# Kernel tuning notes

Hardware: AMD Instinct MI355X
Metric: run time of the kernel (lower is better)

The kernel has to match this reference:

```python
import jax, jax.numpy as jnp
import numpy as np

POS_TH = 0.5
NEG_TH = 0.4
NEGPOS_RATIO = 3
BBOX_ALPHA = 1.5
CONF_ALPHA = 1.0
VAR_CXCY = 0.1
VAR_WH = 0.2
NUM_CLASSES = 41
B, P, G = 8, 100000, 16


def setup_inputs() -> dict:
    key = jax.random.key(0)
    k = jax.random.split(key, 8)
    loc_data = jax.random.normal(k[0], (B, P, 4), dtype=jnp.float32)
    conf_data = jax.random.normal(k[1], (B, P, NUM_CLASSES), dtype=jnp.float32)
    # priors in (cx, cy, w, h), normalized coords
    p_cxy = jax.random.uniform(k[2], (P, 2), minval=0.0, maxval=1.0)
    p_wh = jax.random.uniform(k[3], (P, 2), minval=0.02, maxval=0.3)
    priors = jnp.concatenate([p_cxy, p_wh], axis=1).astype(jnp.float32)
    # gt boxes in point form (x1, y1, x2, y2)
    g_cxy = jax.random.uniform(k[4], (B, G, 2), minval=0.15, maxval=0.85)
    g_wh = jax.random.uniform(k[5], (B, G, 2), minval=0.05, maxval=0.4)
    gt_boxes = jnp.concatenate([
        jnp.clip(g_cxy - g_wh / 2, 0.0, 1.0),
        jnp.clip(g_cxy + g_wh / 2, 0.0, 1.0),
    ], axis=-1).astype(jnp.float32)
    gt_labels = jax.random.randint(k[6], (B, G), 1, NUM_CLASSES)
    return {"loc_data": loc_data, "conf_data": conf_data, "priors": priors,
            "gt_boxes": gt_boxes, "gt_labels": gt_labels}


def point_form(pr):
    return jnp.concatenate([pr[:, :2] - pr[:, 2:] / 2,
                            pr[:, :2] + pr[:, 2:] / 2], axis=1)


def jaccard(a, b):
    # a: [G,4] xyxy, b: [P,4] xyxy -> [G,P]
    lt = jnp.maximum(a[:, None, :2], b[None, :, :2])
    rb = jnp.minimum(a[:, None, 2:], b[None, :, 2:])
    wh = jnp.clip(rb - lt, 0.0)
    inter = wh[..., 0] * wh[..., 1]
    area_a = ((a[:, 2] - a[:, 0]) * (a[:, 3] - a[:, 1]))[:, None]
    area_b = ((b[:, 2] - b[:, 0]) * (b[:, 3] - b[:, 1]))[None, :]
    return inter / (area_a + area_b - inter)


def encode(matched, priors):
    # matched [P,4] xyxy, priors [P,4] cxcywh -> SSD offsets with variances
    g_cxcy = ((matched[:, :2] + matched[:, 2:]) / 2 - priors[:, :2]) / (VAR_CXCY * priors[:, 2:])
    g_wh = jnp.log(jnp.clip((matched[:, 2:] - matched[:, :2]) / priors[:, 2:], 1e-8)) / VAR_WH
    return jnp.concatenate([g_cxcy, g_wh], axis=1)


def match_one(gt_box, gt_label, priors):
    # gt_box [G,4], gt_label [G], priors [P,4] -> loc_t [P,4], conf_t [P]
    pf = point_form(priors)
    ov = jaccard(gt_box, pf)                      # [G,P]
    best_truth_ov = ov.max(axis=0)                # [P]
    best_truth_idx = ov.argmax(axis=0)            # [P]
    best_prior_idx = ov.argmax(axis=1)            # [G] best prior per gt
    # force-match each gt to its best prior
    best_truth_ov = best_truth_ov.at[best_prior_idx].set(2.0)
    best_truth_idx = best_truth_idx.at[best_prior_idx].set(jnp.arange(gt_box.shape[0]))
    conf = gt_label[best_truth_idx]
    conf = jnp.where(best_truth_ov < POS_TH, -1, conf)   # neutral
    conf = jnp.where(best_truth_ov < NEG_TH, 0, conf)    # background
    loc = encode(gt_box[best_truth_idx], priors)
    return loc, conf


def reference(loc_data, conf_data, priors, gt_boxes, gt_labels):
    bsz, n_pri, n_cls = conf_data.shape
    loc_t, conf_t = jax.vmap(match_one, in_axes=(0, 0, None))(gt_boxes, gt_labels, priors)
    pos = conf_t > 0                               # [B,P]
    num_pos = pos.sum(axis=1)                      # [B]
    # pos_weights: uniform 1/num_pos per image (ones split then normalized)
    pos_w = pos.astype(loc_data.dtype) / jnp.clip(num_pos, 1).astype(loc_data.dtype)[:, None]
    # localization: weighted SmoothL1 over positives
    d = loc_data - loc_t
    sl1 = jnp.where(jnp.abs(d) < 1.0, 0.5 * d * d, jnp.abs(d) - 0.5)
    loss_B = (pos_w[..., None] * sl1).sum() * BBOX_ALPHA
    # OHEM hard negative mining on background-suppression loss
    loss_c = jax.nn.logsumexp(conf_data, axis=-1) - conf_data[..., 0]
    loss_c = jnp.where(pos | (conf_t < 0), 0.0, loss_c)
    order = jnp.argsort(-loss_c, axis=1)
    rank = jnp.argsort(order, axis=1)
    num_neg = jnp.clip(NEGPOS_RATIO * num_pos, 0, n_pri - 1)
    neg = (rank < num_neg[:, None]) & (~pos) & (conf_t >= 0)
    keep = (pos | neg).astype(conf_data.dtype)
    logp = jax.nn.log_softmax(conf_data, axis=-1)
    ce = -jnp.take_along_axis(logp, jnp.clip(conf_t, 0)[..., None], axis=-1)[..., 0]
    total_pos = jnp.clip(num_pos.sum(), 1).astype(conf_data.dtype)
    loss_C = (ce * keep).sum() * CONF_ALPHA / total_pos
    return (loss_B + loss_C) / bsz
```

## Files before the change

### kernel.cpp

```cpp
#include <hip/hip_runtime.h>
#include <stdint.h>

#define BATCH 8
#define NPRI 100000
#define NGT 16
#define NCLS 41
#define F_POS_TH 0.5f
#define F_NEG_TH 0.4f

static constexpr int TPB = 256;
static constexpr int MCHUNK = 16;
static constexpr int MLEN = (NPRI + MCHUNK - 1) / MCHUNK;

static constexpr int TILES_PER_B = (NPRI + 63) / 64;
static constexpr int CBLK = (TILES_PER_B + 3) / 4;
static constexpr int CW = 64 * NCLS / 4;
static constexpr int H0BIN = 256;
static constexpr int NBIN = 4096;

static constexpr size_t OFF_KEY  = 0;
static constexpr size_t OFF_GTC  = OFF_KEY + (size_t)BATCH*NPRI*4;
static constexpr size_t OFF_HG   = OFF_GTC + BATCH*NGT*8;
static constexpr size_t OFF_NPOS = OFF_HG + (size_t)BATCH*H0BIN*4;
static constexpr size_t OFF_SL1  = OFF_NPOS + BATCH*4;
static constexpr size_t OFF_CEP  = OFF_SL1  + BATCH*4;
static constexpr size_t OFF_NEG  = OFF_CEP  + BATCH*4;
static constexpr size_t OFF_FTK  = OFF_NEG  + BATCH*4;
static constexpr int ZERO_U32 = (int)((OFF_FTK + 4 - OFF_HG) / 4);

typedef float f32x4 __attribute__((ext_vector_type(4)));

__device__ inline float smoothl1(float d) {
  float a = fabsf(d);
  return a < 1.f ? 0.5f * d * d : a - 0.5f;
}
__device__ inline float aload_f32(const float* p) {
  return __hip_atomic_load(p, __ATOMIC_RELAXED, __HIP_MEMORY_SCOPE_AGENT);
}

__global__ void k_init(unsigned* __restrict__ z, unsigned long long* __restrict__ gtc) {
  int t = threadIdx.x;
  for (int i = t; i < ZERO_U32; i += 512) z[i] = 0u;
  if (t < BATCH * NGT) gtc[t] = 0xFFFFFFFFull;
}

__global__ __launch_bounds__(TPB) void k_match(const float* __restrict__ priors,
                                               const float* __restrict__ gtb,
                                               unsigned long long* __restrict__ gtc) {
  int bg = blockIdx.y;
  int t = threadIdx.x;
  const f32x4 gv = ((const f32x4*)gtb)[bg];
  float garea = (gv[2] - gv[0]) * (gv[3] - gv[1]);
  int pend = min(NPRI, (int)(blockIdx.x + 1) * MLEN);
  unsigned long long best = 0;
  for (int p = blockIdx.x * MLEN + t; p < pend; p += TPB) {
    f32x4 pv = ((const f32x4*)priors)[p];
    float px1 = pv[0] - 0.5f * pv[2], py1 = pv[1] - 0.5f * pv[3];
    float px2 = pv[0] + 0.5f * pv[2], py2 = pv[1] + 0.5f * pv[3];
    float ix = fmaxf(fminf(px2, gv[2]) - fmaxf(px1, gv[0]), 0.f);
    float iy = fmaxf(fminf(py2, gv[3]) - fmaxf(py1, gv[1]), 0.f);
    float inter = ix * iy;
    float parea = (px2 - px1) * (py2 - py1);
    float iou = inter / (parea + garea - inter);
    unsigned long long comp = ((unsigned long long)__float_as_uint(iou) << 32)
                            | (unsigned long long)(0xFFFFFFFFu - (unsigned)p);
    best = best > comp ? best : comp;
  }
#pragma unroll
  for (int off = 32; off; off >>= 1) {
    unsigned long long o = (unsigned long long)__shfl_xor((long long)best, off, 64);
    best = best > o ? best : o;
  }
  __shared__ unsigned long long red[4];
  if ((t & 63) == 0) red[t >> 6] = best;
  __syncthreads();
  if (t == 0) {
    unsigned long long r = red[0];
    r = r > red[1] ? r : red[1];
    r = r > red[2] ? r : red[2];
    r = r > red[3] ? r : red[3];
    atomicMax(&gtc[bg], r);
  }
}

__global__ __launch_bounds__(256, 4) void k_conf(
    const float* __restrict__ loc, const float* __restrict__ conf,
    const float* __restrict__ priors, const float* __restrict__ gtb,
    const int* __restrict__ gtl, const unsigned long long* __restrict__ gtc,
    unsigned* __restrict__ key, unsigned* __restrict__ histg,
    unsigned* __restrict__ npos, float* __restrict__ sl1sum, float* __restrict__ cepos) {
  __shared__ float sums[4][64];
  __shared__ float r0s[4][64];
  __shared__ unsigned hcb[H0BIN];
  __shared__ float redS[4], redC[4]; __shared__ unsigned redP[4];
  const int t = threadIdx.x, w = t >> 6, l = t & 63;
  const int b = blockIdx.y;
  const int tile = blockIdx.x * 4 + w;
  hcb[t] = 0u;
  sums[w][l] = 0.f;
  __syncthreads();
  float accS = 0.f, accC = 0.f; unsigned accP = 0;
  if (tile < TILES_PER_B) {
    const f32x4* c4 = (const f32x4*)conf;
    const size_t base = (size_t)b * (NPRI * NCLS / 4) + (size_t)tile * CW;
    const size_t bend = (size_t)(b + 1) * (NPRI * NCLS / 4) - 1;
    f32x4 rr[11];
#pragma unroll
    for (int u = 0; u < 11; u++) {
      size_t ix = base + (unsigned)(u * 64 + l);
      if (ix > bend) ix = bend;
      rr[u] = c4[ix];
    }
    const int p = tile * 64 + l;
    const bool valid = p < NPRI;
    const int pc = valid ? p : NPRI - 1;
    const f32x4 pv = ((const f32x4*)priors)[pc];
    const f32x4 ld = ((const f32x4*)loc)[(size_t)b * NPRI + pc];
#pragma unroll
    for (int u = 0; u < 11; u++) {
      int cidx = u * 64 + l;
      if (cidx < CW) {
        int f = cidx * 4;
        int r0 = (int)((unsigned)f / 41u);
        int rem = f - r0 * 41;
        float e0 = __expf(rr[u][0]);
        float e1 = __expf(rr[u][1]);
        float e2 = __expf(rr[u][2]);
        float e3 = __expf(rr[u][3]);
        int nlo = 41 - rem;
        float slo = e0, shi = 0.f;
        if (nlo > 1) slo += e1; else shi += e1;
        if (nlo > 2) slo += e2; else shi += e2;
        if (nlo > 3) slo += e3; else shi += e3;
        atomicAdd(&sums[w][r0], slo);
        if (nlo <= 3) atomicAdd(&sums[w][r0 + 1], shi);
        if (rem == 0) r0s[w][r0] = rr[u][0];
        else if (nlo <= 3) {
          float v = (nlo == 1) ? rr[u][1] : (nlo == 2) ? rr[u][2] : rr[u][3];
          r0s[w][r0 + 1] = v;
        }
      }
    }
    float lse = __logf(sums[w][l]);
    float r0v = r0s[w][l];
    if (valid) {
      float px1 = pv[0] - 0.5f * pv[2], py1 = pv[1] - 0.5f * pv[3];
      float px2 = pv[0] + 0.5f * pv[2], py2 = pv[1] + 0.5f * pv[3];
      float parea = (px2 - px1) * (py2 - py1);
      float bov = 0.f; int g = 0;
#pragma unroll
      for (int gg = 0; gg < NGT; gg++) {
        const f32x4 gv = ((const f32x4*)gtb)[b * NGT + gg];
        float ix = fmaxf(fminf(px2, gv[2]) - fmaxf(px1, gv[0]), 0.f);
        float iy = fmaxf(fminf(py2, gv[3]) - fmaxf(py1, gv[1]), 0.f);
        float inter = ix * iy;
        float garea = (gv[2] - gv[0]) * (gv[3] - gv[1]);
        float iou = inter / (parea + garea - inter);
        if (iou > bov) { bov = iou; g = gg; }
      }
      float o = bov;
#pragma unroll
      for (int gg = 0; gg < NGT; gg++) {
        unsigned long long c64 = gtc[b * NGT + gg];
        unsigned pw = 0xFFFFFFFFu - (unsigned)(c64 & 0xFFFFFFFFull);
        if ((unsigned)p == pw) { o = 2.0f; g = gg; }
      }
      int c = gtl[b * NGT + g];
      if (o < F_POS_TH) c = -1;
      if (o < F_NEG_TH) c = 0;
      unsigned kkreg = (c == 0) ? __float_as_uint(lse - r0v) : 0u;
      key[(size_t)b * NPRI + p] = kkreg;
      atomicAdd(&hcb[kkreg >> 24], 1u);
      if (c > 0) {
        accP = 1;
        float rc = conf[((size_t)b * NPRI + p) * NCLS + c];
        accC = lse - rc;
        const f32x4 gvb = ((const f32x4*)gtb)[b * NGT + g];
        float tx = ((gvb[0] + gvb[2]) * 0.5f - pv[0]) / (0.1f * pv[2]);
        float ty = ((gvb[1] + gvb[3]) * 0.5f - pv[1]) / (0.1f * pv[3]);
        float tw = __logf(fmaxf((gvb[2] - gvb[0]) / pv[2], 1e-8f)) / 0.2f;
        float th = __logf(fmaxf((gvb[3] - gvb[1]) / pv[3], 1e-8f)) / 0.2f;
        accS = smoothl1(ld[0] - tx) + smoothl1(ld[1] - ty)
             + smoothl1(ld[2] - tw) + smoothl1(ld[3] - th);
      }
    }
  }
  __syncthreads();
  { unsigned v = hcb[t]; if (v) atomicAdd(&histg[b * H0BIN + t], v); }
  float vs = accS, vc = accC; unsigned vp = accP;
#pragma unroll
  for (int off = 32; off; off >>= 1) {
    vs += __shfl_down(vs, off, 64);
    vc += __shfl_down(vc, off, 64);
    vp += __shfl_down(vp, off, 64);
  }
  if (l == 0) { redS[w] = vs; redC[w] = vc; redP[w] = vp; }
  __syncthreads();
  if (t == 0) {
    float ts = redS[0] + redS[1] + redS[2] + redS[3];
    float tc = redC[0] + redC[1] + redC[2] + redC[3];
    unsigned tp = redP[0] + redP[1] + redP[2] + redP[3];
    if (tp) atomicAdd(&npos[b], tp);
    if (ts != 0.f) atomicAdd(&sl1sum[b], ts);
    if (tc != 0.f) atomicAdd(&cepos[b], tc);
  }
}

__global__ __launch_bounds__(1024) void k_select(
    const unsigned* __restrict__ key, const unsigned* __restrict__ histg,
    const unsigned* __restrict__ npos, const float* __restrict__ sl1sum,
    const float* __restrict__ cepos, float* __restrict__ negsum,
    unsigned* __restrict__ final_tk, float* __restrict__ out) {
  __shared__ unsigned hc[NBIN];
  __shared__ unsigned pcs[256], sc[256];
  __shared__ int wA; __shared__ unsigned kexA;
  __shared__ unsigned kS, prefS;
  __shared__ float redf[16];
  int b = blockIdx.x, t = threadIdx.x;
  unsigned k0 = min(3u * npos[b], (unsigned)(NPRI - 1));
  const int iters = (NPRI + 1023) / 1024;
  if (t < 256) { unsigned v = histg[b * H0BIN + t]; pcs[t] = v; sc[t] = v; }
  if (t == 0) { kS = 0u; prefS = 0u; wA = -1; }
  __syncthreads();
  for (int off = 1; off < 256; off <<= 1) {
    unsigned v = 0;
    if (t < 256) v = (t + off < 256) ? sc[t + off] : 0u;
    __syncthreads();
    if (t < 256) sc[t] += v;
    __syncthreads();
  }
  if (t < 256) {
    unsigned excl = sc[t] - pcs[t];
    if (k0 > 0 && excl < k0 && k0 <= excl + pcs[t]) { wA = t; kexA = excl; }
  }
  __syncthreads();
  if (t == 0 && wA >= 0) { prefS = ((unsigned)wA) << 24; kS = k0 - kexA; }
  __syncthreads();
  for (int lvl = 1; lvl <= 2; lvl++) {
    unsigned k = kS;
    int shift = (lvl == 1) ? 12 : 0;
    int lowcut = (lvl == 1) ? 24 : 12;
    for (int i = t; i < NBIN; i += 1024) hc[i] = 0u;
    if (t == 0) wA = -1;
    __syncthreads();
    unsigned pre = prefS >> lowcut;
    if (k > 0) {
      for (int n = 0; n < iters; n++) {
        int i = n * 1024 + t;
        if (i < NPRI) {
          unsigned kk = key[(size_t)b * NPRI + i];
          if ((kk >> lowcut) == pre) atomicAdd(&hc[(kk >> shift) & 0xFFFu], 1u);
        }
      }
    }
    __syncthreads();
    if (t < 256) {
      unsigned cs = 0;
#pragma unroll
      for (int u = 0; u < 16; u++) cs += hc[t * 16 + u];
      pcs[t] = cs; sc[t] = cs;
    }
    __syncthreads();
    for (int off = 1; off < 256; off <<= 1) {
      unsigned v = 0;
      if (t < 256) v = (t + off < 256) ? sc[t + off] : 0u;
      __syncthreads();
      if (t < 256) sc[t] += v;
      __syncthreads();
    }
    if (t < 256) {
      unsigned excl = sc[t] - pcs[t];
      if (k > 0 && excl < k && k <= excl + pcs[t]) { wA = t; kexA = excl; }
    }
    __syncthreads();
    if (wA >= 0 && t < 64) {
      int w = wA; unsigned exw = kexA;
      unsigned v = (t < 16) ? hc[w * 16 + t] : 0u;
      unsigned sufv = v;
#pragma unroll
      for (int off = 1; off < 16; off <<= 1) {
        unsigned x = __shfl_down(sufv, off, 64);
        if (t + off < 16) sufv += x;
      }
      unsigned excl2 = exw + (sufv - v);
      if (t < 16 && excl2 < k && k <= excl2 + v) {
        prefS |= ((unsigned)(w * 16 + t)) << shift;
        kS = k - excl2;
      }
    }
    __syncthreads();
  }
  unsigned Tu = prefS;
  unsigned tie = kS;
  float acc = 0.f;
  if (k0 > 0) {
    for (int n = 0; n < iters; n++) {
      int i = n * 1024 + t;
      if (i < NPRI) {
        unsigned kk = key[(size_t)b * NPRI + i];
        if (kk > Tu) acc += __uint_as_float(kk);
      }
    }
  }
#pragma unroll
  for (int off = 32; off; off >>= 1) acc += __shfl_down(acc, off, 64);
  if ((t & 63) == 0) redf[t >> 6] = acc;
  __syncthreads();
  if (t == 0) {
    float tot = 0.f;
    for (int wv = 0; wv < 16; wv++) tot += redf[wv];
    if (k0 > 0) tot += (float)tie * __uint_as_float(Tu);
    negsum[b] = tot;
    __threadfence();
    unsigned r2 = atomicAdd(final_tk, 1u);
    if (r2 == BATCH - 1) {
      __threadfence();
      float lb = 0.f, ctot = 0.f; unsigned tp = 0;
      for (int bb = 0; bb < BATCH; bb++) {
        lb += aload_f32(&sl1sum[bb]) / fmaxf((float)npos[bb], 1.f);
        tp += npos[bb];
        ctot += aload_f32(&cepos[bb]) + aload_f32(&negsum[bb]);
      }
      out[0] = (1.5f * lb + ctot / fmaxf((float)tp, 1.f)) / (float)BATCH;
      *final_tk = 0;
    }
  }
}

extern "C" void kernel_launch(void* const* d_in, const int* in_sizes, int n_in,
                              void* d_out, int out_size, void* d_ws, size_t ws_size,
                              hipStream_t stream) {
  const float* loc = (const float*)d_in[0];
  const float* conf = (const float*)d_in[1];
  const float* priors = (const float*)d_in[2];
  const float* gtb = (const float*)d_in[3];
  const int* gtl = (const int*)d_in[4];
  char* ws = (char*)d_ws;
  unsigned* key = (unsigned*)(ws + OFF_KEY);
  unsigned long long* gtc = (unsigned long long*)(ws + OFF_GTC);
  unsigned* histg = (unsigned*)(ws + OFF_HG);
  unsigned* npos = (unsigned*)(ws + OFF_NPOS);
  float* sl1sum = (float*)(ws + OFF_SL1);
  float* cepos = (float*)(ws + OFF_CEP);
  float* negsum = (float*)(ws + OFF_NEG);
  unsigned* final_tk = (unsigned*)(ws + OFF_FTK);
  float* out = (float*)d_out;

  k_init<<<1, 512, 0, stream>>>(histg, gtc);
  dim3 gridM(MCHUNK, BATCH * NGT);
  k_match<<<gridM, TPB, 0, stream>>>(priors, gtb, gtc);
  dim3 gridC(CBLK, BATCH);
  k_conf<<<gridC, 256, 0, stream>>>(loc, conf, priors, gtb, gtl, gtc,
                                    key, histg, npos, sl1sum, cepos);
  k_select<<<BATCH, 1024, 0, stream>>>(key, histg, npos, sl1sum, cepos,
                                       negsum, final_tk, out);
}
```

Baseline: 187.0 us.

## Compute per-prior best overlap once in match kernel and reuse in conf kernel

The match kernel is reorganised to give one thread per prior per image. It computes the IoU against all 16 GT boxes a single time, stores each prior's best overlap and index to a new workspace buffer, and reduces each GT's best prior through shared-memory atomics. The conf kernel then reads this packed value instead of recomputing the 16 IoUs, which removes ALU work from the bandwidth-heavy pass. In exchange, an extra 6.4 MB buffer is written and read. The change also uses wave ballots to aggregate histogram increments for the common bins, relaxes launch bounds to 2 waves per SIMD, and adds a sched_barrier after the conf loads.

```diff
diff --git a/kernel.cpp b/kernel.cpp
--- a/kernel.cpp
+++ b/kernel.cpp
@@ -9,8 +9,7 @@
 #define F_NEG_TH 0.4f
 
 static constexpr int TPB = 256;
-static constexpr int MCHUNK = 16;
-static constexpr int MLEN = (NPRI + MCHUNK - 1) / MCHUNK;
+static constexpr int PBLK = (NPRI + TPB - 1) / TPB;
 
 static constexpr int TILES_PER_B = (NPRI + 63) / 64;
 static constexpr int CBLK = (TILES_PER_B + 3) / 4;
@@ -19,7 +18,8 @@
 static constexpr int NBIN = 4096;
 
 static constexpr size_t OFF_KEY  = 0;
-static constexpr size_t OFF_GTC  = OFF_KEY + (size_t)BATCH*NPRI*4;
+static constexpr size_t OFF_OVBT = OFF_KEY + (size_t)BATCH*NPRI*4;
+static constexpr size_t OFF_GTC  = OFF_OVBT + (size_t)BATCH*NPRI*8;
 static constexpr size_t OFF_HG   = OFF_GTC + BATCH*NGT*8;
 static constexpr size_t OFF_NPOS = OFF_HG + (size_t)BATCH*H0BIN*4;
 static constexpr size_t OFF_SL1  = OFF_NPOS + BATCH*4;
@@ -46,47 +46,48 @@
 
 __global__ __launch_bounds__(TPB) void k_match(const float* __restrict__ priors,
                                                const float* __restrict__ gtb,
+                                               unsigned long long* __restrict__ ovbt,
                                                unsigned long long* __restrict__ gtc) {
-  int bg = blockIdx.y;
+  int b = blockIdx.y;
   int t = threadIdx.x;
-  const f32x4 gv = ((const f32x4*)gtb)[bg];
-  float garea = (gv[2] - gv[0]) * (gv[3] - gv[1]);
-  int pend = min(NPRI, (int)(blockIdx.x + 1) * MLEN);
-  unsigned long long best = 0;
-  for (int p = blockIdx.x * MLEN + t; p < pend; p += TPB) {
-    f32x4 pv = ((const f32x4*)priors)[p];
-    float px1 = pv[0] - 0.5f * pv[2], py1 = pv[1] - 0.5f * pv[3];
-    float px2 = pv[0] + 0.5f * pv[2], py2 = pv[1] + 0.5f * pv[3];
+  int p = blockIdx.x * TPB + t;
+  __shared__ unsigned long long best[NGT];
+  if (t < NGT) best[t] = 0;
+  __syncthreads();
+  bool valid = p < NPRI;
+  int pc = valid ? p : 0;
+  const f32x4 pv = ((const f32x4*)priors)[pc];
+  float px1 = pv[0] - 0.5f * pv[2], py1 = pv[1] - 0.5f * pv[3];
+  float px2 = pv[0] + 0.5f * pv[2], py2 = pv[1] + 0.5f * pv[3];
+  float parea = (px2 - px1) * (py2 - py1);
+  float bov = 0.f; int bidx = 0;
+#pragma unroll
+  for (int g = 0; g < NGT; g++) {
+    const f32x4 gv = ((const f32x4*)gtb)[b * NGT + g];
     float ix = fmaxf(fminf(px2, gv[2]) - fmaxf(px1, gv[0]), 0.f);
     float iy = fmaxf(fminf(py2, gv[3]) - fmaxf(py1, gv[1]), 0.f);
     float inter = ix * iy;
-    float parea = (px2 - px1) * (py2 - py1);
+    float garea = (gv[2] - gv[0]) * (gv[3] - gv[1]);
     float iou = inter / (parea + garea - inter);
-    unsigned long long comp = ((unsigned long long)__float_as_uint(iou) << 32)
-                            | (unsigned long long)(0xFFFFFFFFu - (unsigned)p);
-    best = best > comp ? best : comp;
-  }
-#pragma unroll
-  for (int off = 32; off; off >>= 1) {
-    unsigned long long o = (unsigned long long)__shfl_xor((long long)best, off, 64);
-    best = best > o ? best : o;
-  }
-  __shared__ unsigned long long red[4];
-  if ((t & 63) == 0) red[t >> 6] = best;
-  __syncthreads();
-  if (t == 0) {
-    unsigned long long r = red[0];
-    r = r > red[1] ? r : red[1];
-    r = r > red[2] ? r : red[2];
-    r = r > red[3] ? r : red[3];
-    atomicMax(&gtc[bg], r);
-  }
-}
-
-__global__ __launch_bounds__(256, 4) void k_conf(
+    if (iou > bov) { bov = iou; bidx = g; }
+    if (valid && iou > 0.f) {
+      unsigned long long comp = ((unsigned long long)__float_as_uint(iou) << 32)
+                              | (unsigned long long)(0xFFFFFFFFu - (unsigned)p);
+      if (comp > best[g]) atomicMax(&best[g], comp);
+    }
+  }
+  if (valid)
+    ovbt[(size_t)b * NPRI + p] = ((unsigned long long)__float_as_uint(bov) << 32)
+                               | (unsigned)bidx;
+  __syncthreads();
+  if (t < NGT && best[t] != 0) atomicMax(&gtc[b * NGT + t], best[t]);
+}
+
+__global__ __launch_bounds__(256, 2) void k_conf(
     const float* __restrict__ loc, const float* __restrict__ conf,
     const float* __restrict__ priors, const float* __restrict__ gtb,
     const int* __restrict__ gtl, const unsigned long long* __restrict__ gtc,
+    const unsigned long long* __restrict__ ovbt,
     unsigned* __restrict__ key, unsigned* __restrict__ histg,
     unsigned* __restrict__ npos, float* __restrict__ sl1sum, float* __restrict__ cepos) {
   __shared__ float sums[4][64];
@@ -101,21 +102,23 @@
   __syncthreads();
   float accS = 0.f, accC = 0.f; unsigned accP = 0;
   if (tile < TILES_PER_B) {
-    const f32x4* c4 = (const f32x4*)conf;
-    const size_t base = (size_t)b * (NPRI * NCLS / 4) + (size_t)tile * CW;
-    const size_t bend = (size_t)(b + 1) * (NPRI * NCLS / 4) - 1;
+    const f32x4* c4b = (const f32x4*)conf + (size_t)b * (NPRI * NCLS / 4);
+    const unsigned bend = (unsigned)(NPRI * NCLS / 4 - 1);
+    const unsigned tbase = (unsigned)tile * CW;
     f32x4 rr[11];
 #pragma unroll
     for (int u = 0; u < 11; u++) {
-      size_t ix = base + (unsigned)(u * 64 + l);
-      if (ix > bend) ix = bend;
-      rr[u] = c4[ix];
-    }
+      unsigned ix = tbase + (unsigned)(u * 64 + l);
+      ix = min(ix, bend);
+      rr[u] = c4b[ix];
+    }
+    __builtin_amdgcn_sched_barrier(0);
     const int p = tile * 64 + l;
     const bool valid = p < NPRI;
     const int pc = valid ? p : NPRI - 1;
     const f32x4 pv = ((const f32x4*)priors)[pc];
     const f32x4 ld = ((const f32x4*)loc)[(size_t)b * NPRI + pc];
+    const unsigned long long ob = ovbt[(size_t)b * NPRI + pc];
 #pragma unroll
     for (int u = 0; u < 11; u++) {
       int cidx = u * 64 + l;
@@ -143,22 +146,10 @@
     }
     float lse = __logf(sums[w][l]);
     float r0v = r0s[w][l];
+    unsigned kkreg = 0u;
     if (valid) {
-      float px1 = pv[0] - 0.5f * pv[2], py1 = pv[1] - 0.5f * pv[3];
-      float px2 = pv[0] + 0.5f * pv[2], py2 = pv[1] + 0.5f * pv[3];
-      float parea = (px2 - px1) * (py2 - py1);
-      float bov = 0.f; int g = 0;
-#pragma unroll
-      for (int gg = 0; gg < NGT; gg++) {
-        const f32x4 gv = ((const f32x4*)gtb)[b * NGT + gg];
-        float ix = fmaxf(fminf(px2, gv[2]) - fmaxf(px1, gv[0]), 0.f);
-        float iy = fmaxf(fminf(py2, gv[3]) - fmaxf(py1, gv[1]), 0.f);
-        float inter = ix * iy;
-        float garea = (gv[2] - gv[0]) * (gv[3] - gv[1]);
-        float iou = inter / (parea + garea - inter);
-        if (iou > bov) { bov = iou; g = gg; }
-      }
-      float o = bov;
+      float o = __uint_as_float((unsigned)(ob >> 32));
+      int g = (int)(ob & 0xFFFFull);
 #pragma unroll
       for (int gg = 0; gg < NGT; gg++) {
         unsigned long long c64 = gtc[b * NGT + gg];
@@ -168,9 +159,8 @@
       int c = gtl[b * NGT + g];
       if (o < F_POS_TH) c = -1;
       if (o < F_NEG_TH) c = 0;
-      unsigned kkreg = (c == 0) ? __float_as_uint(lse - r0v) : 0u;
+      kkreg = (c == 0) ? __float_as_uint(lse - r0v) : 0u;
       key[(size_t)b * NPRI + p] = kkreg;
-      atomicAdd(&hcb[kkreg >> 24], 1u);
       if (c > 0) {
         accP = 1;
         float rc = conf[((size_t)b * NPRI + p) * NCLS + c];
@@ -184,6 +174,14 @@
              + smoothl1(ld[2] - tw) + smoothl1(ld[3] - th);
       }
     }
+    unsigned bin = kkreg >> 24;
+    unsigned long long m40 = __ballot(valid && kkreg != 0u && bin == 0x40u);
+    unsigned long long m00 = __ballot(valid && kkreg == 0u);
+    if (m40 && l == __ffsll((long long)m40) - 1)
+      atomicAdd(&hcb[0x40], (unsigned)__popcll(m40));
+    if (m00 && l == __ffsll((long long)m00) - 1)
+      atomicAdd(&hcb[0], (unsigned)__popcll(m00));
+    if (valid && kkreg != 0u && bin != 0x40u) atomicAdd(&hcb[bin], 1u);
   }
   __syncthreads();
   { unsigned v = hcb[t]; if (v) atomicAdd(&histg[b * H0BIN + t], v); }
@@ -337,6 +335,7 @@
   const int* gtl = (const int*)d_in[4];
   char* ws = (char*)d_ws;
   unsigned* key = (unsigned*)(ws + OFF_KEY);
+  unsigned long long* ovbt = (unsigned long long*)(ws + OFF_OVBT);
   unsigned long long* gtc = (unsigned long long*)(ws + OFF_GTC);
   unsigned* histg = (unsigned*)(ws + OFF_HG);
   unsigned* npos = (unsigned*)(ws + OFF_NPOS);
@@ -347,10 +346,10 @@
   float* out = (float*)d_out;
 
   k_init<<<1, 512, 0, stream>>>(histg, gtc);
-  dim3 gridM(MCHUNK, BATCH * NGT);
-  k_match<<<gridM, TPB, 0, stream>>>(priors, gtb, gtc);
+  dim3 gridM(PBLK, BATCH);
+  k_match<<<gridM, TPB, 0, stream>>>(priors, gtb, ovbt, gtc);
   dim3 gridC(CBLK, BATCH);
-  k_conf<<<gridC, 256, 0, stream>>>(loc, conf, priors, gtb, gtl, gtc,
+  k_conf<<<gridC, 256, 0, stream>>>(loc, conf, priors, gtb, gtl, gtc, ovbt,
                                     key, histg, npos, sl1sum, cepos);
   k_select<<<BATCH, 1024, 0, stream>>>(key, histg, npos, sl1sum, cepos,
                                        negsum, final_tk, out);
```

Result: slower. 209.4 us (+12.0%).
